# Kernel optimization log

Measured on AMD Instinct MI355X. Metric: run time of the kernel, lower is better.

## Reference

```python
import jax, jax.numpy as jnp
import numpy as np

N_NODES = 50000
N_EDGES = 1_600_000
IN_F, HID, OUT = 256, 256, 64


def setup_inputs() -> dict:
    key = jax.random.key(0)
    ks = jax.random.split(key, 12)
    inp = {
        "x": jax.random.normal(ks[0], (N_NODES, IN_F), dtype=jnp.float32),
        "src": jax.random.randint(ks[1], (N_EDGES,), 0, N_NODES, dtype=jnp.int32),
        "dst": jax.random.randint(ks[2], (N_EDGES,), 0, N_NODES, dtype=jnp.int32),
        "W_self0": jax.random.normal(ks[3], (IN_F, HID), jnp.float32) * (1.0 / np.sqrt(IN_F)),
        "W_neigh0": jax.random.normal(ks[4], (IN_F, HID), jnp.float32) * (1.0 / np.sqrt(IN_F)),
        "b0": jnp.zeros((HID,), jnp.float32),
        "W_self1": jax.random.normal(ks[5], (HID, HID), jnp.float32) * (1.0 / np.sqrt(HID)),
        "W_neigh1": jax.random.normal(ks[6], (HID, HID), jnp.float32) * (1.0 / np.sqrt(HID)),
        "b1": jnp.zeros((HID,), jnp.float32),
        "W_self2": jax.random.normal(ks[7], (HID, OUT), jnp.float32) * (1.0 / np.sqrt(HID)),
        "W_neigh2": jax.random.normal(ks[8], (HID, OUT), jnp.float32) * (1.0 / np.sqrt(HID)),
        "b2": jnp.zeros((OUT,), jnp.float32),
    }
    return inp


def _sage_conv(h, src, dst, W_self, W_neigh, b, n_nodes):
    # mean aggregator: gather source features along edges, segment-mean at dst
    msg = h[src]                                                    # [E, d]
    agg = jax.ops.segment_sum(msg, dst, num_segments=n_nodes)      # [N, d]
    deg = jax.ops.segment_sum(jnp.ones((src.shape[0],), h.dtype), dst,
                              num_segments=n_nodes)                 # [N]
    h_neigh = agg / jnp.maximum(deg, 1.0)[:, None]
    return h @ W_self + h_neigh @ W_neigh + b


def reference(x, src, dst, W_self0, W_neigh0, b0, W_self1, W_neigh1, b1,
              W_self2, W_neigh2, b2):
    n = x.shape[0]
    # dropout is identity at inference
    h = _sage_conv(x, src, dst, W_self0, W_neigh0, b0, n)
    h = jax.nn.relu(h)
    h = _sage_conv(h, src, dst, W_self1, W_neigh1, b1, n)
    h = jax.nn.relu(h)
    last_non_exiting = h
    h = _sage_conv(h, src, dst, W_self2, W_neigh2, b2, n)
    return (h, last_non_exiting)
```

## Files before the change

kernel.cpp:

```cpp
#include <hip/hip_runtime.h>
#include <hip/hip_bf16.h>
#include <cstdint>


typedef __attribute__((ext_vector_type(8))) short  frag_ab;
typedef __attribute__((ext_vector_type(4))) float  f32x4;
typedef __attribute__((ext_vector_type(2))) float  vf2;

#define BIN_T 4096
#define RSHIFT 9
#define RW 512

__device__ __forceinline__ unsigned short f2b(float f) {
    __hip_bfloat16 h = __float2bfloat16(f);
    return *reinterpret_cast<unsigned short*>(&h);
}
__device__ __forceinline__ unsigned char f2p8(float f) {
    int p = __builtin_amdgcn_cvt_pk_fp8_f32(f, f, 0, false);
    return (unsigned char)(p & 0xff);
}
__device__ __forceinline__ void acc8_v(vf2* a, uint4 v) {
    vf2 t0; t0.x = __uint_as_float(v.x << 16); t0.y = __uint_as_float(v.x & 0xffff0000u);
    vf2 t1; t1.x = __uint_as_float(v.y << 16); t1.y = __uint_as_float(v.y & 0xffff0000u);
    vf2 t2; t2.x = __uint_as_float(v.z << 16); t2.y = __uint_as_float(v.z & 0xffff0000u);
    vf2 t3; t3.x = __uint_as_float(v.w << 16); t3.y = __uint_as_float(v.w & 0xffff0000u);
    a[0] += t0; a[1] += t1; a[2] += t2; a[3] += t3;
}
__device__ __forceinline__ void acc16p_v(vf2* a, uint4 v) {
    a[0] += __builtin_amdgcn_cvt_pk_f32_fp8(v.x, false);
    a[1] += __builtin_amdgcn_cvt_pk_f32_fp8(v.x, true);
    a[2] += __builtin_amdgcn_cvt_pk_f32_fp8(v.y, false);
    a[3] += __builtin_amdgcn_cvt_pk_f32_fp8(v.y, true);
    a[4] += __builtin_amdgcn_cvt_pk_f32_fp8(v.z, false);
    a[5] += __builtin_amdgcn_cvt_pk_f32_fp8(v.z, true);
    a[6] += __builtin_amdgcn_cvt_pk_f32_fp8(v.w, false);
    a[7] += __builtin_amdgcn_cvt_pk_f32_fp8(v.w, true);
}

__device__ __forceinline__ void gl_lds16(const void* g, void* l) {
    __builtin_amdgcn_global_load_lds(
        (const __attribute__((address_space(1))) unsigned int*)g,
        (__attribute__((address_space(3))) unsigned int*)l, 16, 0, 0);
}

__global__ __launch_bounds__(512) void bin_edges(
    const int* __restrict__ src, const int* __restrict__ dst,
    int* __restrict__ bdst, int* __restrict__ bsrc,
    int* __restrict__ gcnt, int E, int cap) {
    __shared__ int lds_d[BIN_T];
    __shared__ int lds_s[BIN_T];
    __shared__ unsigned short lds_b[BIN_T];
    __shared__ int hist[8][128];
    __shared__ int cur[8][128];
    __shared__ int tot[128], scn[128], pref[128], gbase[128];

    const int tid = threadIdx.x;
    const int w = tid >> 6;
    const int e0 = blockIdx.x * BIN_T;
    const int base = e0 + tid * 8;

    int d[8], sv[8], bk[8];
    if (e0 + BIN_T <= E) {
        int4 a0 = *reinterpret_cast<const int4*>(dst + base);
        int4 a1 = *reinterpret_cast<const int4*>(dst + base + 4);
        int4 b0 = *reinterpret_cast<const int4*>(src + base);
        int4 b1 = *reinterpret_cast<const int4*>(src + base + 4);
        d[0] = a0.x; d[1] = a0.y; d[2] = a0.z; d[3] = a0.w;
        d[4] = a1.x; d[5] = a1.y; d[6] = a1.z; d[7] = a1.w;
        sv[0] = b0.x; sv[1] = b0.y; sv[2] = b0.z; sv[3] = b0.w;
        sv[4] = b1.x; sv[5] = b1.y; sv[6] = b1.z; sv[7] = b1.w;
#pragma unroll
        for (int j = 0; j < 8; j++) bk[j] = (int)((unsigned)d[j] >> RSHIFT);
    } else {
#pragma unroll
        for (int j = 0; j < 8; j++) {
            int e = base + j;
            if (e < E) {
                d[j] = dst[e]; sv[j] = src[e];
                bk[j] = (int)((unsigned)d[j] >> RSHIFT);
            } else {
                d[j] = 0; sv[j] = 0; bk[j] = -1;
            }
        }
    }

    for (int i = tid; i < 8 * 128; i += 512) ((int*)hist)[i] = 0;
    __syncthreads();
#pragma unroll
    for (int j = 0; j < 8; j++)
        if (bk[j] >= 0) atomicAdd(&hist[w][bk[j]], 1);
    __syncthreads();
    if (tid < 128) {
        int t = 0;
#pragma unroll
        for (int w2 = 0; w2 < 8; w2++) t += hist[w2][tid];
        tot[tid] = t; scn[tid] = t;
    }
    __syncthreads();
#pragma unroll
    for (int off = 1; off < 128; off <<= 1) {
        int v = 0;
        if (tid < 128 && tid >= off) v = scn[tid - off];
        __syncthreads();
        if (tid < 128 && tid >= off) scn[tid] += v;
        __syncthreads();
    }
    if (tid < 128) {
        pref[tid] = scn[tid] - tot[tid];
        gbase[tid] = atomicAdd(&gcnt[tid], tot[tid]);
        int b0 = pref[tid];
#pragma unroll
        for (int w2 = 0; w2 < 8; w2++) { cur[w2][tid] = b0; b0 += hist[w2][tid]; }
    }
    __syncthreads();
#pragma unroll
    for (int j = 0; j < 8; j++) {
        if (bk[j] >= 0) {
            int pos = atomicAdd(&cur[w][bk[j]], 1);
            lds_d[pos] = d[j];
            lds_s[pos] = sv[j];
            lds_b[pos] = (unsigned short)bk[j];
        }
    }
    __syncthreads();
    const int nv = scn[127];
    for (int i = tid; i < nv; i += 512) {
        int b = lds_b[i];
        int off = gbase[b] + (i - pref[b]);
        bdst[(size_t)b * cap + off] = lds_d[i];
        bsrc[(size_t)b * cap + off] = lds_s[i];
    }
}

__global__ __launch_bounds__(256) void hist_deg(
    const int* __restrict__ bdst, const int* __restrict__ gcnt,
    int* __restrict__ deg, int cap, int N) {
    const int b = blockIdx.x;
    const int cnt = gcnt[b];
    __shared__ int h[RW];
    for (int k = threadIdx.x; k < RW; k += 256) h[k] = 0;
    __syncthreads();
    const int* bd = bdst + (size_t)b * cap;
    for (int i = threadIdx.x; i < cnt; i += 256)
        atomicAdd(&h[bd[i] & (RW - 1)], 1);
    __syncthreads();
    const int v0 = b << RSHIFT;
    for (int k = threadIdx.x; k < RW; k += 256) {
        int node = v0 + k;
        if (node < N) deg[node] = h[k];
    }
}

__global__ __launch_bounds__(256) void scatter_direct(
    const int* __restrict__ bdst, const int* __restrict__ bsrc,
    const int* __restrict__ gcnt, const int* __restrict__ row_start,
    int* __restrict__ csr, int cap, int N) {
    const int b = blockIdx.x;
    const int cnt = gcnt[b];
    const int v0 = b << RSHIFT;
    __shared__ int cur[RW];
    for (int k = threadIdx.x; k < RW; k += 256) {
        int node = v0 + k;
        cur[k] = (node < N) ? row_start[node] : 0;
    }
    __syncthreads();
    const int* bd = bdst + (size_t)b * cap;
    const int* bs = bsrc + (size_t)b * cap;
    for (int i = threadIdx.x; i < cnt; i += 256) {
        int dd = bd[i];
        int ss = bs[i];
        int pos = atomicAdd(&cur[dd & (RW - 1)], 1);
        csr[pos] = ss;
    }
}

__global__ __launch_bounds__(256) void scan_partial_kernel(
    const int* __restrict__ deg, int* __restrict__ partials, int n) {
    const int t = threadIdx.x;
    const int i0 = blockIdx.x * 1024 + t * 4;
    int sum = 0;
#pragma unroll
    for (int j = 0; j < 4; j++) { int i = i0 + j; if (i < n) sum += deg[i]; }
#pragma unroll
    for (int off = 32; off; off >>= 1) sum += __shfl_down(sum, off);
    __shared__ int ws[4];
    int lane = t & 63, wid = t >> 6;
    if (lane == 0) ws[wid] = sum;
    __syncthreads();
    if (t == 0) partials[blockIdx.x] = ws[0] + ws[1] + ws[2] + ws[3];
}

__global__ void scan_partials_kernel(int* __restrict__ p, int nb) {
    const int lane = threadIdx.x;
    int carry = 0;
    for (int base = 0; base < nb; base += 64) {
        int i = base + lane;
        int v = (i < nb) ? p[i] : 0;
        int orig = v;
#pragma unroll
        for (int off = 1; off < 64; off <<= 1) {
            int x = __shfl_up(v, off);
            if (lane >= off) v += x;
        }
        int ex = carry + v - orig;
        if (i < nb) p[i] = ex;
        carry += __shfl(v, 63);
    }
}

__global__ __launch_bounds__(256) void scan_final_kernel(
    const int* __restrict__ deg, const int* __restrict__ pscan,
    int* __restrict__ row_start, int n) {
    const int t = threadIdx.x;
    const int i0 = blockIdx.x * 1024 + t * 4;
    int v0 = (i0 + 0 < n) ? deg[i0 + 0] : 0;
    int v1 = (i0 + 1 < n) ? deg[i0 + 1] : 0;
    int v2 = (i0 + 2 < n) ? deg[i0 + 2] : 0;
    int v3 = (i0 + 3 < n) ? deg[i0 + 3] : 0;
    int tot = v0 + v1 + v2 + v3;
    int lane = t & 63, wid = t >> 6;
    int inc = tot;
#pragma unroll
    for (int off = 1; off < 64; off <<= 1) {
        int x = __shfl_up(inc, off);
        if (lane >= off) inc += x;
    }
    __shared__ int wsum[4];
    if (lane == 63) wsum[wid] = inc;
    __syncthreads();
    int wbase = 0;
    for (int w2 = 0; w2 < wid; w2++) wbase += wsum[w2];
    int r = wbase + inc - tot + pscan[blockIdx.x];
    r += v0; if (i0 + 0 < n) row_start[i0 + 1] = r;
    r += v1; if (i0 + 1 < n) row_start[i0 + 2] = r;
    r += v2; if (i0 + 2 < n) row_start[i0 + 3] = r;
    r += v3; if (i0 + 3 < n) row_start[i0 + 4] = r;
    if (blockIdx.x == 0 && t == 0) row_start[0] = 0;
}

__global__ void conv_x_kernel(const float* __restrict__ in, unsigned short* __restrict__ outb,
                              unsigned char* __restrict__ outp, int n4) {
    int i = blockIdx.x * blockDim.x + threadIdx.x;
    if (i >= n4) return;
    float4 v = *reinterpret_cast<const float4*>(in + (size_t)i * 4);
    ushort4 ob = { f2b(v.x), f2b(v.y), f2b(v.z), f2b(v.w) };
    *reinterpret_cast<ushort4*>(outb + (size_t)i * 4) = ob;
    int p0 = __builtin_amdgcn_cvt_pk_fp8_f32(v.x, v.y, 0, false);
    int p1 = __builtin_amdgcn_cvt_pk_fp8_f32(v.z, v.w, 0, false);
    unsigned int packed = (unsigned int)(p0 & 0xffff) | ((unsigned int)p1 << 16);
    *reinterpret_cast<unsigned int*>(outp + (size_t)i * 4) = packed;
}

__global__ __launch_bounds__(256) void wt_all_kernel(
    const float* __restrict__ Ws0, const float* __restrict__ Wn0,
    const float* __restrict__ Ws1, const float* __restrict__ Wn1,
    const float* __restrict__ Ws2, const float* __restrict__ Wn2,
    unsigned short* __restrict__ Wt0, unsigned short* __restrict__ Wt1,
    unsigned short* __restrict__ Wt2) {
    int b = blockIdx.x;
    const float* W; unsigned short* Wt; int N, koff, Ktot, noff, idx;
    if (b < 1024) {
        int seg = b >> 8; idx = (b & 255) * 256 + threadIdx.x;
        N = 256; Ktot = 512; noff = 0;
        if (seg == 0)      { W = Ws0; Wt = Wt0; koff = 0;   }
        else if (seg == 1) { W = Wn0; Wt = Wt0; koff = 256; }
        else if (seg == 2) { W = Ws1; Wt = Wt1; koff = 0;   }
        else               { W = Wn1; Wt = Wt1; koff = 256; }
    } else {
        int seg = (b - 1024) >> 6; idx = ((b - 1024) & 63) * 256 + threadIdx.x;
        N = 64; Ktot = 256; koff = 0;
        if (seg == 0) { W = Ws2; Wt = Wt2; noff = 0;  }
        else          { W = Wn2; Wt = Wt2; noff = 64; }
    }
    int k = idx / N, n = idx - k * N;
    Wt[(size_t)(n + noff) * Ktot + koff + k] = f2b(W[(size_t)idx]);
}

__global__ __launch_bounds__(256) void agg256_fp8(
    const unsigned char* __restrict__ hsrc, const int* __restrict__ row_start,
    const int* __restrict__ csr, unsigned short* __restrict__ out, int n) {
    int wv = (blockIdx.x * blockDim.x + threadIdx.x) >> 6;
    int lane = threadIdx.x & 63;
    if (wv >= n) return;
    int s0 = row_start[wv], s1 = row_start[wv + 1];
    int deg = s1 - s0;
    const int q  = lane >> 4;
    const int li = lane & 15;
    vf2 a[8];
#pragma unroll
    for (int k = 0; k < 8; k++) a[k] = (vf2)(0.f);

    uint4 v[4];
#pragma unroll
    for (int j = 0; j < 4; j++) {
        int e = s0 + q + 4 * j;
        int idx = csr[e < s1 ? e : s1 - 1];
        v[j] = make_uint4(0u, 0u, 0u, 0u);
        if (e < s1)
            v[j] = *reinterpret_cast<const uint4*>(hsrc + (size_t)idx * 256 + li * 16);
    }
    for (int base = s0 + 16; base < s1; base += 16) {
        uint4 nv[4];
#pragma unroll
        for (int j = 0; j < 4; j++) {
            int e = base + q + 4 * j;
            int idx = csr[e < s1 ? e : s1 - 1];
            nv[j] = make_uint4(0u, 0u, 0u, 0u);
            if (e < s1)
                nv[j] = *reinterpret_cast<const uint4*>(hsrc + (size_t)idx * 256 + li * 16);
        }
#pragma unroll
        for (int j = 0; j < 4; j++) acc16p_v(a, v[j]);
#pragma unroll
        for (int j = 0; j < 4; j++) v[j] = nv[j];
    }
#pragma unroll
    for (int j = 0; j < 4; j++) acc16p_v(a, v[j]);

    float af[16];
#pragma unroll
    for (int p = 0; p < 8; p++) { af[2 * p] = a[p].x; af[2 * p + 1] = a[p].y; }
#pragma unroll
    for (int k = 0; k < 16; k++) {
        af[k] += __shfl_xor(af[k], 16);
        af[k] += __shfl_xor(af[k], 32);
    }
    if (q == 0) {
        float sc = 1.0f / (float)max(deg, 1);
        uint4 o0, o1;
        o0.x = ((unsigned)f2b(af[1]  * sc) << 16) | f2b(af[0]  * sc);
        o0.y = ((unsigned)f2b(af[3]  * sc) << 16) | f2b(af[2]  * sc);
        o0.z = ((unsigned)f2b(af[5]  * sc) << 16) | f2b(af[4]  * sc);
        o0.w = ((unsigned)f2b(af[7]  * sc) << 16) | f2b(af[6]  * sc);
        o1.x = ((unsigned)f2b(af[9]  * sc) << 16) | f2b(af[8]  * sc);
        o1.y = ((unsigned)f2b(af[11] * sc) << 16) | f2b(af[10] * sc);
        o1.z = ((unsigned)f2b(af[13] * sc) << 16) | f2b(af[12] * sc);
        o1.w = ((unsigned)f2b(af[15] * sc) << 16) | f2b(af[14] * sc);
        *reinterpret_cast<uint4*>(out + (size_t)wv * 256 + li * 16) = o0;
        *reinterpret_cast<uint4*>(out + (size_t)wv * 256 + li * 16 + 8) = o1;
    }
}

__global__ __launch_bounds__(256) void agg64_final(
    const unsigned short* __restrict__ t, const int* __restrict__ row_start,
    const int* __restrict__ csr, const float* __restrict__ Sself,
    const float* __restrict__ b2, float* __restrict__ h2, int n) {
    int wv = (blockIdx.x * blockDim.x + threadIdx.x) >> 6;
    int lane = threadIdx.x & 63;
    if (wv >= n) return;
    int s0 = row_start[wv], s1 = row_start[wv + 1];
    int deg = s1 - s0;
    const int g  = lane >> 3;
    const int li = lane & 7;
    vf2 a[4];
#pragma unroll
    for (int k = 0; k < 4; k++) a[k] = (vf2)(0.f);

    int base = s0 + g;
    const bool have = base < s1;
    uint4 v0 = make_uint4(0u, 0u, 0u, 0u), v1 = v0;
    if (have) {
        int i0 = csr[base];
        v0 = *reinterpret_cast<const uint4*>(t + (size_t)i0 * 64 + li * 8);
        int e1 = base + 8;
        if (e1 < s1) {
            int i1 = csr[e1];
            v1 = *reinterpret_cast<const uint4*>(t + (size_t)i1 * 64 + li * 8);
        }
    }
    for (base += 16; base < s1; base += 16) {
        uint4 n0, n1 = make_uint4(0u, 0u, 0u, 0u);
        {
            int i0 = csr[base];
            n0 = *reinterpret_cast<const uint4*>(t + (size_t)i0 * 64 + li * 8);
            int e1 = base + 8;
            if (e1 < s1) {
                int i1 = csr[e1];
                n1 = *reinterpret_cast<const uint4*>(t + (size_t)i1 * 64 + li * 8);
            }
        }
        acc8_v(a, v0); acc8_v(a, v1);
        v0 = n0; v1 = n1;
    }
    if (have) { acc8_v(a, v0); acc8_v(a, v1); }

    float af[8];
#pragma unroll
    for (int p = 0; p < 4; p++) { af[2 * p] = a[p].x; af[2 * p + 1] = a[p].y; }
#pragma unroll
    for (int k = 0; k < 8; k++) {
        af[k] += __shfl_xor(af[k], 8);
        af[k] += __shfl_xor(af[k], 16);
        af[k] += __shfl_xor(af[k], 32);
    }
    if (g == 0) {
        float sc = 1.0f / (float)max(deg, 1);
        float4 s0v = *reinterpret_cast<const float4*>(Sself + (size_t)wv * 64 + li * 8);
        float4 s1v = *reinterpret_cast<const float4*>(Sself + (size_t)wv * 64 + li * 8 + 4);
        float4 bb0 = *reinterpret_cast<const float4*>(b2 + li * 8);
        float4 bb1 = *reinterpret_cast<const float4*>(b2 + li * 8 + 4);
        float4 o0 = make_float4(s0v.x + af[0] * sc + bb0.x, s0v.y + af[1] * sc + bb0.y,
                                s0v.z + af[2] * sc + bb0.z, s0v.w + af[3] * sc + bb0.w);
        float4 o1 = make_float4(s1v.x + af[4] * sc + bb1.x, s1v.y + af[5] * sc + bb1.y,
                                s1v.z + af[6] * sc + bb1.z, s1v.w + af[7] * sc + bb1.w);
        *reinterpret_cast<float4*>(h2 + (size_t)wv * 64 + li * 8) = o0;
        *reinterpret_cast<float4*>(h2 + (size_t)wv * 64 + li * 8 + 4) = o1;
    }
}

#define BTM 128
#define BTN 256
#define BTK 32

__global__ __launch_bounds__(512, 4) void gemm_big512(
    const unsigned short* __restrict__ A, const unsigned short* __restrict__ G,
    const unsigned short* __restrict__ Wt, const float* __restrict__ bias,
    float* __restrict__ outF, unsigned short* __restrict__ outB,
    unsigned char* __restrict__ outP, int M) {
    __shared__ unsigned short Asb[BTM][BTK];
    __shared__ unsigned short Bsb[BTN][BTK];

    const int tid = threadIdx.x;
    const int row0 = blockIdx.x * BTM;
    const int w = tid >> 6, lane = tid & 63;
    const int mw = (w & 1) * 64;
    const int nw = (w >> 1) * 64;
    const int lm = lane & 15, lq = lane >> 4;
    const int lr = lane >> 2;
    const int lc = (lane & 3) * 8;

    f32x4 acc[4][4];
#pragma unroll
    for (int i = 0; i < 4; i++)
#pragma unroll
        for (int j = 0; j < 4; j++) acc[i][j] = (f32x4)(0.f);

    for (int k0 = 0; k0 < 512; k0 += BTK) {
        const unsigned short* __restrict__ Ap = (k0 >= 256) ? G : A;
        const int kl = k0 & 255;
        {
            int gr = row0 + w * 16 + lr;
            if (gr < M)
                gl_lds16(Ap + (size_t)gr * 256 + kl + lc, &Asb[w * 16][0]);
        }
#pragma unroll
        for (int h = 0; h < 2; ++h) {
            int gn = w * 32 + h * 16 + lr;
            gl_lds16(Wt + (size_t)gn * 512 + k0 + lc, &Bsb[w * 32 + h * 16][0]);
        }
        __syncthreads();

        frag_ab a[4], b[4];
#pragma unroll
        for (int i = 0; i < 4; i++)
            a[i] = *reinterpret_cast<const frag_ab*>(&Asb[mw + i * 16 + lm][lq * 8]);
#pragma unroll
        for (int j = 0; j < 4; j++)
            b[j] = *reinterpret_cast<const frag_ab*>(&Bsb[nw + j * 16 + lm][lq * 8]);
#pragma unroll
        for (int i = 0; i < 4; i++)
#pragma unroll
            for (int j = 0; j < 4; j++)
                acc[i][j] = __builtin_amdgcn_mfma_f32_16x16x32_bf16(a[i], b[j], acc[i][j], 0, 0, 0);
        __syncthreads();
    }

#pragma unroll
    for (int i = 0; i < 4; i++) {
#pragma unroll
        for (int j = 0; j < 4; j++) {
            int cg = nw + j * 16 + lm;
#pragma unroll
            for (int r = 0; r < 4; r++) {
                int rg = row0 + mw + i * 16 + lq * 4 + r;
                if (rg >= M) continue;
                float v = acc[i][j][r] + bias[cg];
                v = fmaxf(v, 0.f);
                outB[(size_t)rg * 256 + cg] = f2b(v);
                if (outF) outF[(size_t)rg * 256 + cg] = v;
                if (outP) outP[(size_t)rg * 256 + cg] = f2p8(v);
            }
        }
    }
}

#define TM 128
#define TN 64
#define TK 32

__global__ __launch_bounds__(256) void gemm_mfma(
    const unsigned short* __restrict__ A, const unsigned short* __restrict__ Wt,
    float* __restrict__ outF, unsigned short* __restrict__ outB, int M) {
    __shared__ unsigned short Asb[TM][TK];
    __shared__ unsigned short Bsb[TN][TK];

    const int tid = threadIdx.x;
    const int row0 = blockIdx.x * TM;
    const int col0 = blockIdx.y * TN;

    const int w = tid >> 6, lane = tid & 63;
    const int mw = (w & 1) * 64;
    const int nw = (w >> 1) * 32;
    const int lm = lane & 15, lq = lane >> 4;
    const int lr = lane >> 2;
    const int lc = (lane & 3) * 8;

    f32x4 acc[4][2];
#pragma unroll
    for (int i = 0; i < 4; i++)
#pragma unroll
        for (int j = 0; j < 2; j++) acc[i][j] = (f32x4)(0.f);

    for (int k0 = 0; k0 < 256; k0 += TK) {
#pragma unroll
        for (int h = 0; h < 2; ++h) {
            int r16 = w * 32 + h * 16;
            int gr = row0 + r16 + lr;
            if (gr < M)
                gl_lds16(A + (size_t)gr * 256 + k0 + lc, &Asb[r16][0]);
        }
        {
            int n16 = w * 16;
            int gn = col0 + n16 + lr;
            gl_lds16(Wt + (size_t)gn * 256 + k0 + lc, &Bsb[n16][0]);
        }
        __syncthreads();

        frag_ab a[4], b[2];
#pragma unroll
        for (int i = 0; i < 4; i++)
            a[i] = *reinterpret_cast<const frag_ab*>(&Asb[mw + i * 16 + lm][lq * 8]);
#pragma unroll
        for (int j = 0; j < 2; j++)
            b[j] = *reinterpret_cast<const frag_ab*>(&Bsb[nw + j * 16 + lm][lq * 8]);
#pragma unroll
        for (int i = 0; i < 4; i++)
#pragma unroll
            for (int j = 0; j < 2; j++)
                acc[i][j] = __builtin_amdgcn_mfma_f32_16x16x32_bf16(a[i], b[j], acc[i][j], 0, 0, 0);
        __syncthreads();
    }

#pragma unroll
    for (int i = 0; i < 4; i++) {
#pragma unroll
        for (int j = 0; j < 2; j++) {
            int c = nw + j * 16 + lm;
#pragma unroll
            for (int r = 0; r < 4; r++) {
                int rg = row0 + mw + i * 16 + lq * 4 + r;
                if (rg >= M) continue;
                float v = acc[i][j][r];
                if (col0 == 0) outF[(size_t)rg * 64 + c] = v;
                else           outB[(size_t)rg * 64 + c] = f2b(v);
            }
        }
    }
}

extern "C" void kernel_launch(void* const* d_in, const int* in_sizes, int n_in,
                              void* d_out, int out_size, void* d_ws, size_t ws_size,
                              hipStream_t stream) {
    const float* x   = (const float*)d_in[0];
    const int*   src = (const int*)d_in[1];
    const int*   dst = (const int*)d_in[2];
    const float* Ws0 = (const float*)d_in[3];
    const float* Wn0 = (const float*)d_in[4];
    const float* b0  = (const float*)d_in[5];
    const float* Ws1 = (const float*)d_in[6];
    const float* Wn1 = (const float*)d_in[7];
    const float* b1  = (const float*)d_in[8];
    const float* Ws2 = (const float*)d_in[9];
    const float* Wn2 = (const float*)d_in[10];
    const float* b2  = (const float*)d_in[11];

    const int N = in_sizes[0] / 256;
    const int E = in_sizes[1];

    float* out = (float*)d_out;
    float* h2 = out;
    float* h1 = out + (size_t)N * 64;

    const int nbuk = (N + RW - 1) >> RSHIFT;
    const int cap  = (E + nbuk - 1) / nbuk + 2048;

    char* w = (char*)d_ws;
    auto align16 = [](char* p) { return (char*)(((uintptr_t)p + 15) & ~(uintptr_t)15); };
    int* deg       = (int*)w;  w += (size_t)N * 4;
    int* gcnt      = (int*)w;  w += 128 * 4;
    int* row_start = (int*)w;  w += (size_t)(N + 1) * 4;
    int* partials  = (int*)w;  w += 256 * 4;
    int* csr       = (int*)w;  w += (size_t)E * 4;
    int* bdst      = (int*)w;  w += (size_t)nbuk * cap * 4;
    int* bsrc      = (int*)w;  w += (size_t)nbuk * cap * 4;
    w = align16(w);
    unsigned short* Wt0   = (unsigned short*)w; w += (size_t)256 * 512 * 2;
    unsigned short* Wt1   = (unsigned short*)w; w += (size_t)256 * 512 * 2;
    unsigned short* Wt2   = (unsigned short*)w; w += (size_t)128 * 256 * 2;
    w = align16(w);
    unsigned short* xb    = (unsigned short*)w; w += (size_t)N * 256 * 2;
    unsigned short* A1b   = (unsigned short*)w; w += (size_t)N * 256 * 2;
    unsigned short* H0b   = (unsigned short*)w; w += (size_t)N * 256 * 2;
    unsigned short* h1b   = (unsigned short*)w; w += (size_t)N * 256 * 2;
    unsigned char* x8  = (unsigned char*)H0b;
    unsigned char* H08 = (unsigned char*)h1b;
    unsigned short* Tb    = xb;
    float*          Sself = (float*)A1b;

    const int nb = (N + 1023) / 1024;

    hipMemsetAsync(gcnt, 0, 128 * 4, stream);
    bin_edges<<<(E + BIN_T - 1) / BIN_T, 512, 0, stream>>>(src, dst, bdst, bsrc, gcnt, E, cap);
    hist_deg<<<nbuk, 256, 0, stream>>>(bdst, gcnt, deg, cap, N);
    scan_partial_kernel<<<nb, 256, 0, stream>>>(deg, partials, N);
    scan_partials_kernel<<<1, 64, 0, stream>>>(partials, nb);
    scan_final_kernel<<<nb, 256, 0, stream>>>(deg, partials, row_start, N);
    scatter_direct<<<nbuk, 256, 0, stream>>>(bdst, bsrc, gcnt, row_start, csr, cap, N);

    {
        int n4 = N * 256 / 4;
        conv_x_kernel<<<(n4 + 255) / 256, 256, 0, stream>>>(x, xb, x8, n4);
    }
    wt_all_kernel<<<1152, 256, 0, stream>>>(Ws0, Wn0, Ws1, Wn1, Ws2, Wn2, Wt0, Wt1, Wt2);

    dim3 aggGrid((N + 3) / 4);
    dim3 gStripe((N + BTM - 1) / BTM);
    dim3 gL2((N + TM - 1) / TM, 2);

    agg256_fp8<<<aggGrid, 256, 0, stream>>>(x8, row_start, csr, A1b, N);
    gemm_big512<<<gStripe, 512, 0, stream>>>(xb, A1b, Wt0, b0, nullptr, H0b, H08, N);
    agg256_fp8<<<aggGrid, 256, 0, stream>>>(H08, row_start, csr, A1b, N);
    gemm_big512<<<gStripe, 512, 0, stream>>>(H0b, A1b, Wt1, b1, h1, h1b, nullptr, N);
    gemm_mfma<<<gL2, 256, 0, stream>>>(h1b, Wt2, Sself, Tb, N);
    agg64_final<<<aggGrid, 256, 0, stream>>>(Tb, row_start, csr, Sself, b2, h2, N);
}
```

Baseline: 436.8 us.

## Assign multiple nodes per wave in aggregation kernels with zero-row padding

The aggregation kernels now give each 16-lane (or 8-lane) group its own destination node instead of splitting one node's edges across the whole wave. This removes the cross-lane shuffle reduction, and a sentinel zero row at index N replaces per-edge branch masking. The loop runs to the wave's maximum degree with a 6-deep rolling prefetch, which wastes loads on shorter-degree nodes. Buffers are enlarged by one row and zeroed by extra memsets to hold the padding row.

```diff
diff --git a/kernel.cpp b/kernel.cpp
--- a/kernel.cpp
+++ b/kernel.cpp
@@ -278,133 +278,114 @@
 
 __global__ __launch_bounds__(256) void agg256_fp8(
     const unsigned char* __restrict__ hsrc, const int* __restrict__ row_start,
-    const int* __restrict__ csr, unsigned short* __restrict__ out, int n) {
+    const int* __restrict__ csr, unsigned short* __restrict__ out, int n, int zrow) {
     int wv = (blockIdx.x * blockDim.x + threadIdx.x) >> 6;
     int lane = threadIdx.x & 63;
-    if (wv >= n) return;
-    int s0 = row_start[wv], s1 = row_start[wv + 1];
-    int deg = s1 - s0;
+    if (wv * 4 >= n) return;
     const int q  = lane >> 4;
     const int li = lane & 15;
+    const int node = wv * 4 + q;
+    const bool act = node < n;
+    int s0 = act ? row_start[node] : 0;
+    int s1 = act ? row_start[node + 1] : 0;
+    int deg = s1 - s0;
+    int nmax = deg;
+    nmax = max(nmax, __shfl_xor(nmax, 16));
+    nmax = max(nmax, __shfl_xor(nmax, 32));
+
+    const size_t lioff = (size_t)li * 16;
     vf2 a[8];
 #pragma unroll
     for (int k = 0; k < 8; k++) a[k] = (vf2)(0.f);
 
-    uint4 v[4];
-#pragma unroll
-    for (int j = 0; j < 4; j++) {
-        int e = s0 + q + 4 * j;
-        int idx = csr[e < s1 ? e : s1 - 1];
-        v[j] = make_uint4(0u, 0u, 0u, 0u);
-        if (e < s1)
-            v[j] = *reinterpret_cast<const uint4*>(hsrc + (size_t)idx * 256 + li * 16);
-    }
-    for (int base = s0 + 16; base < s1; base += 16) {
-        uint4 nv[4];
-#pragma unroll
-        for (int j = 0; j < 4; j++) {
-            int e = base + q + 4 * j;
-            int idx = csr[e < s1 ? e : s1 - 1];
-            nv[j] = make_uint4(0u, 0u, 0u, 0u);
-            if (e < s1)
-                nv[j] = *reinterpret_cast<const uint4*>(hsrc + (size_t)idx * 256 + li * 16);
-        }
-#pragma unroll
-        for (int j = 0; j < 4; j++) acc16p_v(a, v[j]);
-#pragma unroll
-        for (int j = 0; j < 4; j++) v[j] = nv[j];
-    }
-#pragma unroll
-    for (int j = 0; j < 4; j++) acc16p_v(a, v[j]);
-
-    float af[16];
-#pragma unroll
-    for (int p = 0; p < 8; p++) { af[2 * p] = a[p].x; af[2 * p + 1] = a[p].y; }
-#pragma unroll
-    for (int k = 0; k < 16; k++) {
-        af[k] += __shfl_xor(af[k], 16);
-        af[k] += __shfl_xor(af[k], 32);
-    }
-    if (q == 0) {
+#define LD256(vv, k) { int _e = s0 + (k); \
+    int _ci = csr[max(min(_e, s1 - 1), 0)]; \
+    int _ii = ((k) < deg) ? _ci : zrow; \
+    vv = *reinterpret_cast<const uint4*>(hsrc + (size_t)_ii * 256 + lioff); }
+
+    uint4 v0, v1, v2, v3, v4, v5;
+    LD256(v0, 0); LD256(v1, 1); LD256(v2, 2);
+    LD256(v3, 3); LD256(v4, 4); LD256(v5, 5);
+    for (int b = 0; b < nmax; b += 6) {
+        acc16p_v(a, v0); LD256(v0, b + 6);
+        acc16p_v(a, v1); LD256(v1, b + 7);
+        acc16p_v(a, v2); LD256(v2, b + 8);
+        acc16p_v(a, v3); LD256(v3, b + 9);
+        acc16p_v(a, v4); LD256(v4, b + 10);
+        acc16p_v(a, v5); LD256(v5, b + 11);
+    }
+#undef LD256
+
+    if (act) {
         float sc = 1.0f / (float)max(deg, 1);
         uint4 o0, o1;
-        o0.x = ((unsigned)f2b(af[1]  * sc) << 16) | f2b(af[0]  * sc);
-        o0.y = ((unsigned)f2b(af[3]  * sc) << 16) | f2b(af[2]  * sc);
-        o0.z = ((unsigned)f2b(af[5]  * sc) << 16) | f2b(af[4]  * sc);
-        o0.w = ((unsigned)f2b(af[7]  * sc) << 16) | f2b(af[6]  * sc);
-        o1.x = ((unsigned)f2b(af[9]  * sc) << 16) | f2b(af[8]  * sc);
-        o1.y = ((unsigned)f2b(af[11] * sc) << 16) | f2b(af[10] * sc);
-        o1.z = ((unsigned)f2b(af[13] * sc) << 16) | f2b(af[12] * sc);
-        o1.w = ((unsigned)f2b(af[15] * sc) << 16) | f2b(af[14] * sc);
-        *reinterpret_cast<uint4*>(out + (size_t)wv * 256 + li * 16) = o0;
-        *reinterpret_cast<uint4*>(out + (size_t)wv * 256 + li * 16 + 8) = o1;
+        o0.x = ((unsigned)f2b(a[0].y * sc) << 16) | f2b(a[0].x * sc);
+        o0.y = ((unsigned)f2b(a[1].y * sc) << 16) | f2b(a[1].x * sc);
+        o0.z = ((unsigned)f2b(a[2].y * sc) << 16) | f2b(a[2].x * sc);
+        o0.w = ((unsigned)f2b(a[3].y * sc) << 16) | f2b(a[3].x * sc);
+        o1.x = ((unsigned)f2b(a[4].y * sc) << 16) | f2b(a[4].x * sc);
+        o1.y = ((unsigned)f2b(a[5].y * sc) << 16) | f2b(a[5].x * sc);
+        o1.z = ((unsigned)f2b(a[6].y * sc) << 16) | f2b(a[6].x * sc);
+        o1.w = ((unsigned)f2b(a[7].y * sc) << 16) | f2b(a[7].x * sc);
+        *reinterpret_cast<uint4*>(out + (size_t)node * 256 + li * 16) = o0;
+        *reinterpret_cast<uint4*>(out + (size_t)node * 256 + li * 16 + 8) = o1;
     }
 }
 
 __global__ __launch_bounds__(256) void agg64_final(
     const unsigned short* __restrict__ t, const int* __restrict__ row_start,
     const int* __restrict__ csr, const float* __restrict__ Sself,
-    const float* __restrict__ b2, float* __restrict__ h2, int n) {
+    const float* __restrict__ b2, float* __restrict__ h2, int n, int zrow) {
     int wv = (blockIdx.x * blockDim.x + threadIdx.x) >> 6;
     int lane = threadIdx.x & 63;
-    if (wv >= n) return;
-    int s0 = row_start[wv], s1 = row_start[wv + 1];
-    int deg = s1 - s0;
+    if (wv * 8 >= n) return;
     const int g  = lane >> 3;
     const int li = lane & 7;
+    const int node = wv * 8 + g;
+    const bool act = node < n;
+    int s0 = act ? row_start[node] : 0;
+    int s1 = act ? row_start[node + 1] : 0;
+    int deg = s1 - s0;
+    int nmax = deg;
+    nmax = max(nmax, __shfl_xor(nmax, 8));
+    nmax = max(nmax, __shfl_xor(nmax, 16));
+    nmax = max(nmax, __shfl_xor(nmax, 32));
+
+    const size_t lioff = (size_t)li * 8;
     vf2 a[4];
 #pragma unroll
     for (int k = 0; k < 4; k++) a[k] = (vf2)(0.f);
 
-    int base = s0 + g;
-    const bool have = base < s1;
-    uint4 v0 = make_uint4(0u, 0u, 0u, 0u), v1 = v0;
-    if (have) {
-        int i0 = csr[base];
-        v0 = *reinterpret_cast<const uint4*>(t + (size_t)i0 * 64 + li * 8);
-        int e1 = base + 8;
-        if (e1 < s1) {
-            int i1 = csr[e1];
-            v1 = *reinterpret_cast<const uint4*>(t + (size_t)i1 * 64 + li * 8);
-        }
-    }
-    for (base += 16; base < s1; base += 16) {
-        uint4 n0, n1 = make_uint4(0u, 0u, 0u, 0u);
-        {
-            int i0 = csr[base];
-            n0 = *reinterpret_cast<const uint4*>(t + (size_t)i0 * 64 + li * 8);
-            int e1 = base + 8;
-            if (e1 < s1) {
-                int i1 = csr[e1];
-                n1 = *reinterpret_cast<const uint4*>(t + (size_t)i1 * 64 + li * 8);
-            }
-        }
-        acc8_v(a, v0); acc8_v(a, v1);
-        v0 = n0; v1 = n1;
-    }
-    if (have) { acc8_v(a, v0); acc8_v(a, v1); }
-
-    float af[8];
-#pragma unroll
-    for (int p = 0; p < 4; p++) { af[2 * p] = a[p].x; af[2 * p + 1] = a[p].y; }
-#pragma unroll
-    for (int k = 0; k < 8; k++) {
-        af[k] += __shfl_xor(af[k], 8);
-        af[k] += __shfl_xor(af[k], 16);
-        af[k] += __shfl_xor(af[k], 32);
-    }
-    if (g == 0) {
+#define LD64(vv, k) { int _e = s0 + (k); \
+    int _ci = csr[max(min(_e, s1 - 1), 0)]; \
+    int _ii = ((k) < deg) ? _ci : zrow; \
+    vv = *reinterpret_cast<const uint4*>(t + (size_t)_ii * 64 + lioff); }
+
+    uint4 v0, v1, v2, v3, v4, v5;
+    LD64(v0, 0); LD64(v1, 1); LD64(v2, 2);
+    LD64(v3, 3); LD64(v4, 4); LD64(v5, 5);
+    for (int b = 0; b < nmax; b += 6) {
+        acc8_v(a, v0); LD64(v0, b + 6);
+        acc8_v(a, v1); LD64(v1, b + 7);
+        acc8_v(a, v2); LD64(v2, b + 8);
+        acc8_v(a, v3); LD64(v3, b + 9);
+        acc8_v(a, v4); LD64(v4, b + 10);
+        acc8_v(a, v5); LD64(v5, b + 11);
+    }
+#undef LD64
+
+    if (act) {
         float sc = 1.0f / (float)max(deg, 1);
-        float4 s0v = *reinterpret_cast<const float4*>(Sself + (size_t)wv * 64 + li * 8);
-        float4 s1v = *reinterpret_cast<const float4*>(Sself + (size_t)wv * 64 + li * 8 + 4);
+        float4 s0v = *reinterpret_cast<const float4*>(Sself + (size_t)node * 64 + li * 8);
+        float4 s1v = *reinterpret_cast<const float4*>(Sself + (size_t)node * 64 + li * 8 + 4);
         float4 bb0 = *reinterpret_cast<const float4*>(b2 + li * 8);
         float4 bb1 = *reinterpret_cast<const float4*>(b2 + li * 8 + 4);
-        float4 o0 = make_float4(s0v.x + af[0] * sc + bb0.x, s0v.y + af[1] * sc + bb0.y,
-                                s0v.z + af[2] * sc + bb0.z, s0v.w + af[3] * sc + bb0.w);
-        float4 o1 = make_float4(s1v.x + af[4] * sc + bb1.x, s1v.y + af[5] * sc + bb1.y,
-                                s1v.z + af[6] * sc + bb1.z, s1v.w + af[7] * sc + bb1.w);
-        *reinterpret_cast<float4*>(h2 + (size_t)wv * 64 + li * 8) = o0;
-        *reinterpret_cast<float4*>(h2 + (size_t)wv * 64 + li * 8 + 4) = o1;
+        float4 o0 = make_float4(s0v.x + a[0].x * sc + bb0.x, s0v.y + a[0].y * sc + bb0.y,
+                                s0v.z + a[1].x * sc + bb0.z, s0v.w + a[1].y * sc + bb0.w);
+        float4 o1 = make_float4(s1v.x + a[2].x * sc + bb1.x, s1v.y + a[2].y * sc + bb1.y,
+                                s1v.z + a[3].x * sc + bb1.z, s1v.w + a[3].y * sc + bb1.w);
+        *reinterpret_cast<float4*>(h2 + (size_t)node * 64 + li * 8) = o0;
+        *reinterpret_cast<float4*>(h2 + (size_t)node * 64 + li * 8 + 4) = o1;
     }
 }
 
@@ -598,10 +579,10 @@
     unsigned short* Wt1   = (unsigned short*)w; w += (size_t)256 * 512 * 2;
     unsigned short* Wt2   = (unsigned short*)w; w += (size_t)128 * 256 * 2;
     w = align16(w);
-    unsigned short* xb    = (unsigned short*)w; w += (size_t)N * 256 * 2;
+    unsigned short* xb    = (unsigned short*)w; w += (size_t)(N + 1) * 256 * 2;
     unsigned short* A1b   = (unsigned short*)w; w += (size_t)N * 256 * 2;
-    unsigned short* H0b   = (unsigned short*)w; w += (size_t)N * 256 * 2;
-    unsigned short* h1b   = (unsigned short*)w; w += (size_t)N * 256 * 2;
+    unsigned short* H0b   = (unsigned short*)w; w += (size_t)(N + 1) * 256 * 2;
+    unsigned short* h1b   = (unsigned short*)w; w += (size_t)(N + 1) * 256 * 2;
     unsigned char* x8  = (unsigned char*)H0b;
     unsigned char* H08 = (unsigned char*)h1b;
     unsigned short* Tb    = xb;
@@ -623,14 +604,19 @@
     }
     wt_all_kernel<<<1152, 256, 0, stream>>>(Ws0, Wn0, Ws1, Wn1, Ws2, Wn2, Wt0, Wt1, Wt2);
 
-    dim3 aggGrid((N + 3) / 4);
+    hipMemsetAsync(x8  + (size_t)N * 256, 0, 256, stream);
+    hipMemsetAsync(H08 + (size_t)N * 256, 0, 256, stream);
+
+    dim3 agg256Grid((N + 15) / 16);
+    dim3 agg64Grid((N + 31) / 32);
     dim3 gStripe((N + BTM - 1) / BTM);
     dim3 gL2((N + TM - 1) / TM, 2);
 
-    agg256_fp8<<<aggGrid, 256, 0, stream>>>(x8, row_start, csr, A1b, N);
+    agg256_fp8<<<agg256Grid, 256, 0, stream>>>(x8, row_start, csr, A1b, N, N);
     gemm_big512<<<gStripe, 512, 0, stream>>>(xb, A1b, Wt0, b0, nullptr, H0b, H08, N);
-    agg256_fp8<<<aggGrid, 256, 0, stream>>>(H08, row_start, csr, A1b, N);
+    hipMemsetAsync((char*)Tb + (size_t)N * 128, 0, 128, stream);
+    agg256_fp8<<<agg256Grid, 256, 0, stream>>>(H08, row_start, csr, A1b, N, N);
     gemm_big512<<<gStripe, 512, 0, stream>>>(H0b, A1b, Wt1, b1, h1, h1b, nullptr, N);
     gemm_mfma<<<gL2, 256, 0, stream>>>(h1b, Wt2, Sself, Tb, N);
-    agg64_final<<<aggGrid, 256, 0, stream>>>(Tb, row_start, csr, Sself, b2, h2, N);
-}
+    agg64_final<<<agg64Grid, 256, 0, stream>>>(Tb, row_start, csr, Sself, b2, h2, N, N);
+}
```

Result: no change. 445.1 us (+1.9%).
